# Kernel tuning notes

Measured on AMD Instinct MI355X. Metric: run time of the kernel, lower is better.

The kernel has to match this reference:

```python
import jax, jax.numpy as jnp
import numpy as np

H = 16          # num_heads
NB = 32         # pos_bias_num_buckets
EPS = 1e-8      # RMSNorm eps


def setup_inputs() -> dict:
    key = jax.random.key(0)
    ks = jax.random.split(key, 8)
    B, L, K, R, M, Dm, Dq = 2, 32, 2, 64, 128, 2048, 2048
    x = jax.random.normal(ks[0], (B, L, K, R, Dm), jnp.float32)
    past_ca_hidden_states = jax.random.normal(ks[1], (B, L, M, Dm), jnp.float32)
    past_ca_attention_mask = jax.random.bernoulli(ks[2], 0.95, (B, L, M)).astype(jnp.float32)
    ln_scale = jnp.ones((Dm,), jnp.float32)
    q_w = jax.random.normal(ks[3], (Dq, Dm), jnp.float32) * 0.02      # torch Linear weight [out,in]
    kv_w = jax.random.normal(ks[4], (2 * Dq, Dm), jnp.float32) * 0.02
    out_w = jax.random.normal(ks[5], (Dm, Dq), jnp.float32) * 0.02
    bias_table = jax.random.normal(ks[6], (NB, H), jnp.float32) * 0.02  # relative_attention_bias.weight
    return dict(x=x, past_ca_hidden_states=past_ca_hidden_states,
                past_ca_attention_mask=past_ca_attention_mask,
                ln_scale=ln_scale, q_w=q_w, kv_w=kv_w, out_w=out_w,
                bias_table=bias_table)


def _rel_bias(bias_table, r, m):
    # linear bucketing, bidirectional=True (RelativePositionBias._relative_position_bucket_linear)
    mn = -(NB // 2) - (NB % 2 - 1)   # -15 for NB=32
    mx = NB // 2                      # 16
    rel = jnp.arange(m)[None, :] - jnp.arange(r)[:, None]   # memory - query, [r, m]
    buckets = jnp.clip(rel, mn, mx) - mn                    # in [0, NB)
    return jnp.transpose(bias_table[buckets], (2, 0, 1))    # [H, r, m]


def reference(x, past_ca_hidden_states, past_ca_attention_mask,
              ln_scale, q_w, kv_w, out_w, bias_table):
    B, L, K, R, Dm = x.shape
    M = past_ca_hidden_states.shape[2]
    Dq = q_w.shape[0]
    dh = Dq // H

    # RMSNorm (p=-1: full norm)
    rms = jnp.linalg.norm(x, axis=-1, keepdims=True) * (Dm ** -0.5)
    xn = (x / (rms + EPS)) * ln_scale

    # projections (no bias)
    q = jnp.einsum('blkrc,qc->blkrq', xn, q_w)                 # [B,L,K,R,Dq]
    kv = jnp.einsum('blmc,qc->blmq', past_ca_hidden_states, kv_w)  # [B,L,M,2Dq]
    k = kv[..., :Dq]
    v = kv[..., Dq:]

    # split heads
    q = q.reshape(B, L, K, R, H, dh).transpose(0, 1, 2, 4, 3, 5)  # [B,L,K,H,R,dh]
    k = k.reshape(B, L, M, H, dh).transpose(0, 1, 3, 2, 4)        # [B,L,H,M,dh]
    v = v.reshape(B, L, M, H, dh).transpose(0, 1, 3, 2, 4)        # [B,L,H,M,dh]

    # NOTE: original applies NO 1/sqrt(dh) scaling
    scores = jnp.einsum('blkhrd,blhmd->blkhrm', q, k)             # [B,L,K,H,R,M]
    scores = scores + _rel_bias(bias_table, R, M)                 # broadcast [H,R,M]
    mask_add = (1.0 - past_ca_attention_mask) * -10000.0          # [B,L,M]
    scores = scores + mask_add[:, :, None, None, None, :]

    attn = jax.nn.softmax(scores, axis=-1)
    out = jnp.einsum('blkhrm,blhmd->blkhrd', attn, v)             # [B,L,K,H,R,dh]
    out = out.transpose(0, 1, 2, 4, 3, 5).reshape(B, L, K, R, Dq)  # merge heads '(h d)'
    out = jnp.einsum('blkrq,cq->blkrc', out, out_w)                # final_proj
    return out + x, attn
```

## Files before the change

### kernel.cpp

```cpp
#include <hip/hip_runtime.h>

typedef _Float16 f16;
typedef _Float16 f16x8 __attribute__((ext_vector_type(8)));
typedef float f32x4 __attribute__((ext_vector_type(4)));

#define LDS_GL16(g, l) __builtin_amdgcn_global_load_lds( \
    (const __attribute__((address_space(1))) void*)(g),  \
    (__attribute__((address_space(3))) void*)(l), 16, 0, 0)

__global__ __launch_bounds__(256) void conv_kern(const float* __restrict__ in,
                                                 f16* __restrict__ out, int n8) {
    int i = blockIdx.x * 256 + threadIdx.x;
    if (i >= n8) return;
    long o = (long)i * 8;
    float4 a = *(const float4*)(in + o);
    float4 b = *(const float4*)(in + o + 4);
    f16x8 v = { (f16)a.x,(f16)a.y,(f16)a.z,(f16)a.w,
                (f16)b.x,(f16)b.y,(f16)b.z,(f16)b.w };
    *(f16x8*)(out + o) = v;
}

__global__ __launch_bounds__(256) void rmsnorm_kern(const float* __restrict__ x,
                                                    const float* __restrict__ scale,
                                                    f16* __restrict__ out) {
    long base = (long)blockIdx.x * 2048 + threadIdx.x * 8;
    float4 a = *(const float4*)(x + base);
    float4 b = *(const float4*)(x + base + 4);
    float ss = a.x*a.x + a.y*a.y + a.z*a.z + a.w*a.w
             + b.x*b.x + b.y*b.y + b.z*b.z + b.w*b.w;
    #pragma unroll
    for (int d = 1; d < 64; d <<= 1) ss += __shfl_xor(ss, d, 64);
    __shared__ float red[4];
    if ((threadIdx.x & 63) == 0) red[threadIdx.x >> 6] = ss;
    __syncthreads();
    ss = red[0] + red[1] + red[2] + red[3];
    float inv = 1.0f / (sqrtf(ss * (1.0f / 2048.0f)) + 1e-8f);
    int c = threadIdx.x * 8;
    float4 s1 = *(const float4*)(scale + c);
    float4 s2 = *(const float4*)(scale + c + 4);
    f16x8 v = { (f16)(a.x*inv*s1.x),(f16)(a.y*inv*s1.y),(f16)(a.z*inv*s1.z),(f16)(a.w*inv*s1.w),
                (f16)(b.x*inv*s2.x),(f16)(b.y*inv*s2.y),(f16)(b.z*inv*s2.z),(f16)(b.w*inv*s2.w) };
    *(f16x8*)(out + base) = v;
}

template<int EPI>
__global__ __launch_bounds__(512, 2) void gemm256(
        const f16* __restrict__ A, const f16* __restrict__ B,
        f16* __restrict__ Ch, float* __restrict__ Cf,
        const float* __restrict__ resid, int M, int N, int Kd) {
    alignas(16) __shared__ f16 lds[65536];
    int nbx = N >> 8;
    int cpx = gridDim.x >> 3;
    int fid = (blockIdx.x & 7) * cpx + (blockIdx.x >> 3);
    int by = fid / nbx, bx = fid % nbx;
    int m0 = by << 8, n0 = bx << 8;
    int tid = threadIdx.x, lane = tid & 63, wid = tid >> 6;
    int wm = wid >> 2, wn = wid & 3, bh = wn >> 1;
    int lr = lane & 15, g = lane >> 4;

    long offA[4], offB[4]; int dA[4], dB[4];
    {
        int o16a = wn * 64 + lane;
        int o16b = ((wm << 1) | (wn & 1)) * 64 + lane;
        #pragma unroll
        for (int rd = 0; rd < 4; ++rd) {
            int oa = rd * 256 + o16a;
            int ra = wm * 128 + (oa >> 3);
            offA[rd] = (long)(m0 + ra) * Kd + (((lane & 7) ^ (ra & 7)) << 3);
            dA[rd] = wm * 8192 + oa * 8;
            int ob = rd * 256 + o16b;
            int rb = bh * 128 + (ob >> 3);
            offB[rd] = (long)(n0 + rb) * Kd + (((lane & 7) ^ (rb & 7)) << 3);
            dB[rd] = bh * 8192 + ob * 8;
        }
    }
    auto stage = [&](int kt, int p) {
        const f16* Ak = A + kt * 64;
        const f16* Bk = B + kt * 64;
        f16* la = lds + p * 16384;
        f16* lb = lds + 32768 + p * 16384;
        #pragma unroll
        for (int rd = 0; rd < 4; ++rd) {
            LDS_GL16(Ak + offA[rd], la + dA[rd]);
            LDS_GL16(Bk + offB[rd], lb + dB[rd]);
        }
    };

    f32x4 acc[8][4] = {};
    int NT = Kd >> 6;
    stage(0, 0);
    stage(1, 1);
    for (int t = 0; t < NT; ++t) {
        int p = t & 1;
        if (t + 1 < NT) asm volatile("s_waitcnt vmcnt(8)" ::: "memory");
        else            asm volatile("s_waitcnt vmcnt(0)" ::: "memory");
        __builtin_amdgcn_s_barrier();
        const f16* Ap = lds + p * 16384;
        const f16* Bp = lds + 32768 + p * 16384;
        f16x8 bf[2][4];
        #pragma unroll
        for (int kk = 0; kk < 2; ++kk)
            #pragma unroll
            for (int j = 0; j < 4; ++j) {
                int row = wn * 64 + j * 16 + lr;
                int c8 = (kk * 4 + g) ^ (row & 7);
                bf[kk][j] = *(const f16x8*)(Bp + row * 64 + c8 * 8);
            }
        #pragma unroll
        for (int q = 0; q < 4; ++q) {
            f16x8 af[2][2];
            #pragma unroll
            for (int kk = 0; kk < 2; ++kk)
                #pragma unroll
                for (int ii = 0; ii < 2; ++ii) {
                    int row = wm * 128 + (q * 2 + ii) * 16 + lr;
                    int c8 = (kk * 4 + g) ^ (row & 7);
                    af[kk][ii] = *(const f16x8*)(Ap + row * 64 + c8 * 8);
                }
            __builtin_amdgcn_s_setprio(1);
            #pragma unroll
            for (int ii = 0; ii < 2; ++ii)
                #pragma unroll
                for (int j = 0; j < 4; ++j)
                    #pragma unroll
                    for (int kk = 0; kk < 2; ++kk)
                        acc[q * 2 + ii][j] = __builtin_amdgcn_mfma_f32_16x16x32_f16(
                            af[kk][ii], bf[kk][j], acc[q * 2 + ii][j], 0, 0, 0);
            __builtin_amdgcn_s_setprio(0);
        }
        __builtin_amdgcn_s_barrier();
        if (t + 2 < NT) stage(t + 2, p);
    }
    #pragma unroll
    for (int i = 0; i < 8; ++i) {
        #pragma unroll
        for (int j = 0; j < 4; ++j) {
            #pragma unroll
            for (int reg = 0; reg < 4; ++reg) {
                int row = m0 + wm * 128 + i * 16 + g * 4 + reg;
                int col = n0 + wn * 64 + j * 16 + lr;
                long idx = (long)row * N + col;
                float v = acc[i][j][reg];
                if (EPI == 0) Ch[idx] = (f16)v;
                else          Cf[idx] = v + resid[idx];
            }
        }
    }
}

__global__ __launch_bounds__(256, 2) void attn_kern(
        const f16* __restrict__ Q,
        const f16* __restrict__ KV,
        const float* __restrict__ mask,
        const float* __restrict__ bias,
        float* __restrict__ attn_out,
        f16* __restrict__ pv_out) {
    __shared__ f16 Vs[128 * 128];
    __shared__ f16 P[64 * 136];
    int blk = blockIdx.x;
    int h  = blk & 15;
    int bk = blk >> 4;
    int bl = bk >> 1;
    int tid = threadIdx.x, lane = tid & 63, w = tid >> 6;
    int r0 = w << 4;
    int lr = lane & 15, g = lane >> 4;
    long qbase  = (long)bk * 64 * 2048;
    long kvbase = (long)bl * 128 * 4096;
    const f16* vsrc = KV + kvbase + 2048 + h * 128;
    {
        int idx = tid;
        #pragma unroll
        for (int rnd = 0; rnd < 8; ++rnd) {
            int vrow = idx >> 4, c = idx & 15;
            LDS_GL16(vsrc + (long)vrow * 4096 + c * 8, Vs + idx * 8);
            idx += 256;
        }
    }
    f16x8 aq[4];
    const f16* qrow = Q + qbase + (long)(r0 + lr) * 2048 + h * 128 + g * 8;
    #pragma unroll
    for (int t4 = 0; t4 < 4; ++t4) aq[t4] = *(const f16x8*)(qrow + t4 * 32);
    f32x4 s[8] = {};
    const f16* kbase = KV + kvbase + h * 128 + g * 8;
    #pragma unroll
    for (int j = 0; j < 8; ++j) {
        #pragma unroll
        for (int t4 = 0; t4 < 4; ++t4) {
            f16x8 bkf = *(const f16x8*)(kbase + (long)(j * 16 + lr) * 4096 + t4 * 32);
            s[j] = __builtin_amdgcn_mfma_f32_16x16x32_f16(aq[t4], bkf, s[j], 0, 0, 0);
        }
    }
    float madd[8];
    #pragma unroll
    for (int j = 0; j < 8; ++j)
        madd[j] = (1.0f - mask[(long)bl * 128 + j * 16 + lr]) * -10000.0f;
    #pragma unroll
    for (int reg = 0; reg < 4; ++reg) {
        int r = r0 + g * 4 + reg;
        float mx = -3.0e38f;
        #pragma unroll
        for (int j = 0; j < 8; ++j) {
            int m = j * 16 + lr;
            int rel = m - r;
            int bkt = (rel < -15 ? -15 : (rel > 16 ? 16 : rel)) + 15;
            float v = s[j][reg] + bias[bkt * 16 + h] + madd[j];
            s[j][reg] = v;
            mx = fmaxf(mx, v);
        }
        #pragma unroll
        for (int d = 1; d < 16; d <<= 1) mx = fmaxf(mx, __shfl_xor(mx, d, 64));
        float sum = 0.0f;
        #pragma unroll
        for (int j = 0; j < 8; ++j) {
            float e = __expf(s[j][reg] - mx);
            s[j][reg] = e;
            sum += e;
        }
        #pragma unroll
        for (int d = 1; d < 16; d <<= 1) sum += __shfl_xor(sum, d, 64);
        float inv = 1.0f / sum;
        #pragma unroll
        for (int j = 0; j < 8; ++j) s[j][reg] *= inv;
    }
    long abase = (long)blk * 64 * 128;
    #pragma unroll
    for (int reg = 0; reg < 4; ++reg) {
        int r = r0 + g * 4 + reg;
        #pragma unroll
        for (int j = 0; j < 8; ++j) {
            attn_out[abase + (long)r * 128 + j * 16 + lr] = s[j][reg];
            P[r * 136 + j * 16 + lr] = (f16)s[j][reg];
        }
    }
    __syncthreads();
    f16x8 pa[4];
    #pragma unroll
    for (int t4 = 0; t4 < 4; ++t4)
        pa[t4] = *(const f16x8*)(P + (r0 + lr) * 136 + t4 * 32 + g * 8);
    f32x4 o[8] = {};
    #pragma unroll
    for (int dj = 0; dj < 8; ++dj) {
        #pragma unroll
        for (int t4 = 0; t4 < 4; ++t4) {
            f16x8 bv;
            #pragma unroll
            for (int rg = 0; rg < 8; ++rg)
                bv[rg] = Vs[(t4 * 32 + g * 8 + rg) * 128 + dj * 16 + lr];
            o[dj] = __builtin_amdgcn_mfma_f32_16x16x32_f16(pa[t4], bv, o[dj], 0, 0, 0);
        }
    }
    f16* ob = pv_out + qbase + h * 128;
    #pragma unroll
    for (int dj = 0; dj < 8; ++dj)
        #pragma unroll
        for (int reg = 0; reg < 4; ++reg)
            ob[(long)(r0 + g * 4 + reg) * 2048 + dj * 16 + lr] = (f16)o[dj][reg];
}

extern "C" void kernel_launch(void* const* d_in, const int* in_sizes, int n_in,
                              void* d_out, int out_size, void* d_ws, size_t ws_size,
                              hipStream_t stream) {
    const float* x     = (const float*)d_in[0];
    const float* hid   = (const float*)d_in[1];
    const float* mask  = (const float*)d_in[2];
    const float* lnsc  = (const float*)d_in[3];
    const float* q_w   = (const float*)d_in[4];
    const float* kv_w  = (const float*)d_in[5];
    const float* out_w = (const float*)d_in[6];
    const float* bias  = (const float*)d_in[7];
    float* out0 = (float*)d_out;
    float* attn = out0 + 16777216;

    f16* kv_h  = (f16*)out0;
    f16* xn_h  = (f16*)attn;
    f16* hid_h = (f16*)(attn + 8388608);
    char* ws = (char*)d_ws;
    f16* q_h    = (f16*)(ws);
    f16* ao_h   = (f16*)(ws + 33554432L);
    f16* qw_h   = (f16*)(ws + 67108864L);
    f16* kvw_h  = (f16*)(ws + 75497472L);
    f16* outw_h = (f16*)(ws + 92274688L);

    conv_kern<<<2048, 256, 0, stream>>>(q_w,   qw_h,   524288);
    conv_kern<<<4096, 256, 0, stream>>>(kv_w,  kvw_h, 1048576);
    conv_kern<<<2048, 256, 0, stream>>>(out_w, outw_h, 524288);
    conv_kern<<<8192, 256, 0, stream>>>(hid,   hid_h, 2097152);
    rmsnorm_kern<<<8192, 256, 0, stream>>>(x, lnsc, xn_h);
    gemm256<0><<<256, 512, 0, stream>>>(xn_h, qw_h, q_h, nullptr, nullptr,
                                        8192, 2048, 2048);
    gemm256<0><<<512, 512, 0, stream>>>(hid_h, kvw_h, kv_h, nullptr, nullptr,
                                        8192, 4096, 2048);
    attn_kern<<<2048, 256, 0, stream>>>(q_h, kv_h, mask, bias, attn, ao_h);
    gemm256<1><<<256, 512, 0, stream>>>(ao_h, outw_h, nullptr, out0, x,
                                        8192, 2048, 2048);
}
```

Baseline: 424.4 us.

## Restructure GEMM main loop into 8-phase interleaved load/MFMA schedule

Rewrites the 256x256 GEMM main loop so each K-tile is split into quarter stages of global->LDS loads, interleaved with register-fragment loads and MFMA clusters across 8 barrier-separated phases per two K-tiles. This follows the HipKittens-style 8-wave ping-pong schedule and is meant to hide global and LDS latency behind matrix math. The price is many more barriers and a fixed-count vmcnt discipline, with a hand-written tail that assumes an even number of K-tiles.

```diff
diff --git a/kernel.cpp b/kernel.cpp
--- a/kernel.cpp
+++ b/kernel.cpp
@@ -7,6 +7,8 @@
 #define LDS_GL16(g, l) __builtin_amdgcn_global_load_lds( \
     (const __attribute__((address_space(1))) void*)(g),  \
     (__attribute__((address_space(3))) void*)(l), 16, 0, 0)
+#define VMCNT(N) asm volatile("s_waitcnt vmcnt(" #N ")" ::: "memory")
+#define BAR() __builtin_amdgcn_s_barrier()
 
 __global__ __launch_bounds__(256) void conv_kern(const float* __restrict__ in,
                                                  f16* __restrict__ out, int n8) {
@@ -54,83 +56,113 @@
     int fid = (blockIdx.x & 7) * cpx + (blockIdx.x >> 3);
     int by = fid / nbx, bx = fid % nbx;
     int m0 = by << 8, n0 = bx << 8;
-    int tid = threadIdx.x, lane = tid & 63, wid = tid >> 6;
-    int wm = wid >> 2, wn = wid & 3, bh = wn >> 1;
+    int tid = threadIdx.x, lane = tid & 63;
+    int wid = tid >> 6, wm = wid >> 2, wn = wid & 3;
     int lr = lane & 15, g = lane >> 4;
-
-    long offA[4], offB[4]; int dA[4], dB[4];
+    int iL = tid >> 3, cb = tid & 7;
+
+    auto stage = [&](int kt, int p, int r) {
+        #pragma unroll
+        for (int rnd = 0; rnd < 2; ++rnd) {
+            if (r == 0 || r == 3) {
+                int row = iL + rnd * 128 + (r == 3 ? 64 : 0);
+                LDS_GL16(A + (long)(m0 + row) * Kd + kt * 64 + ((cb ^ (row & 7)) << 3),
+                         lds + p * 16384 + row * 64 + (cb << 3));
+            } else {
+                int row = (iL & 31) + ((iL >> 5) + rnd * 2) * 64 + (r == 2 ? 32 : 0);
+                LDS_GL16(B + (long)(n0 + row) * Kd + kt * 64 + ((cb ^ (row & 7)) << 3),
+                         lds + 32768 + p * 16384 + row * 64 + (cb << 3));
+            }
+        }
+    };
+
+    f32x4 acc[8][4] = {};
+    f16x8 a[4][2], b0[2][2], b1[2][2];
+
+    auto loadA = [&](const f16* bp, int qm) {
+        #pragma unroll
+        for (int mf = 0; mf < 4; ++mf) {
+            int row = wm * 128 + (qm * 4 + mf) * 16 + lr;
+            #pragma unroll
+            for (int kk = 0; kk < 2; ++kk)
+                a[mf][kk] = *(const f16x8*)(bp + row * 64 + (((kk * 4 + g) ^ (row & 7)) << 3));
+        }
+    };
+    auto loadB = [&](f16x8 (&d)[2][2], const f16* bp, int qn) {
+        #pragma unroll
+        for (int nf = 0; nf < 2; ++nf) {
+            int row = wn * 64 + (qn * 2 + nf) * 16 + lr;
+            #pragma unroll
+            for (int kk = 0; kk < 2; ++kk)
+                d[nf][kk] = *(const f16x8*)(bp + row * 64 + (((kk * 4 + g) ^ (row & 7)) << 3));
+        }
+    };
+    auto mma = [&](f16x8 (&bb)[2][2], int qm, int qn) {
+        __builtin_amdgcn_s_setprio(1);
+        #pragma unroll
+        for (int mf = 0; mf < 4; ++mf)
+            #pragma unroll
+            for (int nf = 0; nf < 2; ++nf)
+                #pragma unroll
+                for (int kk = 0; kk < 2; ++kk)
+                    acc[qm * 4 + mf][qn * 2 + nf] = __builtin_amdgcn_mfma_f32_16x16x32_f16(
+                        a[mf][kk], bb[nf][kk], acc[qm * 4 + mf][qn * 2 + nf], 0, 0, 0);
+        __builtin_amdgcn_s_setprio(0);
+    };
+
+    const f16* A0p = lds;
+    const f16* A1p = lds + 16384;
+    const f16* B0p = lds + 32768;
+    const f16* B1p = lds + 49152;
+    int NT = Kd >> 6, NI = NT >> 1;
+
+    stage(0, 0, 0); stage(0, 0, 1); stage(0, 0, 2); stage(0, 0, 3);
+    stage(1, 1, 0); stage(1, 1, 1); stage(1, 1, 2);
+    VMCNT(6); BAR();
+
+    for (int it = 0; it < NI - 1; ++it) {
+        int t0 = it * 2;
+        loadA(A0p, 0); loadB(b0, B0p, 0);
+        stage(t0 + 1, 1, 3);
+        VMCNT(6); BAR(); mma(b0, 0, 0); BAR();
+        loadB(b1, B0p, 1);
+        stage(t0 + 2, 0, 0);
+        VMCNT(6); BAR(); mma(b1, 0, 1); BAR();
+        loadA(A0p, 1);
+        stage(t0 + 2, 0, 1);
+        VMCNT(6); BAR(); mma(b1, 1, 1); BAR();
+        stage(t0 + 2, 0, 2);
+        VMCNT(6); BAR(); mma(b0, 1, 0); BAR();
+        loadA(A1p, 0); loadB(b0, B1p, 0);
+        stage(t0 + 2, 0, 3);
+        VMCNT(6); BAR(); mma(b0, 0, 0); BAR();
+        loadB(b1, B1p, 1);
+        stage(t0 + 3, 1, 0);
+        VMCNT(6); BAR(); mma(b1, 0, 1); BAR();
+        loadA(A1p, 1);
+        stage(t0 + 3, 1, 1);
+        VMCNT(6); BAR(); mma(b1, 1, 1); BAR();
+        stage(t0 + 3, 1, 2);
+        VMCNT(6); BAR(); mma(b0, 1, 0); BAR();
+    }
     {
-        int o16a = wn * 64 + lane;
-        int o16b = ((wm << 1) | (wn & 1)) * 64 + lane;
-        #pragma unroll
-        for (int rd = 0; rd < 4; ++rd) {
-            int oa = rd * 256 + o16a;
-            int ra = wm * 128 + (oa >> 3);
-            offA[rd] = (long)(m0 + ra) * Kd + (((lane & 7) ^ (ra & 7)) << 3);
-            dA[rd] = wm * 8192 + oa * 8;
-            int ob = rd * 256 + o16b;
-            int rb = bh * 128 + (ob >> 3);
-            offB[rd] = (long)(n0 + rb) * Kd + (((lane & 7) ^ (rb & 7)) << 3);
-            dB[rd] = bh * 8192 + ob * 8;
-        }
-    }
-    auto stage = [&](int kt, int p) {
-        const f16* Ak = A + kt * 64;
-        const f16* Bk = B + kt * 64;
-        f16* la = lds + p * 16384;
-        f16* lb = lds + 32768 + p * 16384;
-        #pragma unroll
-        for (int rd = 0; rd < 4; ++rd) {
-            LDS_GL16(Ak + offA[rd], la + dA[rd]);
-            LDS_GL16(Bk + offB[rd], lb + dB[rd]);
-        }
-    };
-
-    f32x4 acc[8][4] = {};
-    int NT = Kd >> 6;
-    stage(0, 0);
-    stage(1, 1);
-    for (int t = 0; t < NT; ++t) {
-        int p = t & 1;
-        if (t + 1 < NT) asm volatile("s_waitcnt vmcnt(8)" ::: "memory");
-        else            asm volatile("s_waitcnt vmcnt(0)" ::: "memory");
-        __builtin_amdgcn_s_barrier();
-        const f16* Ap = lds + p * 16384;
-        const f16* Bp = lds + 32768 + p * 16384;
-        f16x8 bf[2][4];
-        #pragma unroll
-        for (int kk = 0; kk < 2; ++kk)
-            #pragma unroll
-            for (int j = 0; j < 4; ++j) {
-                int row = wn * 64 + j * 16 + lr;
-                int c8 = (kk * 4 + g) ^ (row & 7);
-                bf[kk][j] = *(const f16x8*)(Bp + row * 64 + c8 * 8);
-            }
-        #pragma unroll
-        for (int q = 0; q < 4; ++q) {
-            f16x8 af[2][2];
-            #pragma unroll
-            for (int kk = 0; kk < 2; ++kk)
-                #pragma unroll
-                for (int ii = 0; ii < 2; ++ii) {
-                    int row = wm * 128 + (q * 2 + ii) * 16 + lr;
-                    int c8 = (kk * 4 + g) ^ (row & 7);
-                    af[kk][ii] = *(const f16x8*)(Ap + row * 64 + c8 * 8);
-                }
-            __builtin_amdgcn_s_setprio(1);
-            #pragma unroll
-            for (int ii = 0; ii < 2; ++ii)
-                #pragma unroll
-                for (int j = 0; j < 4; ++j)
-                    #pragma unroll
-                    for (int kk = 0; kk < 2; ++kk)
-                        acc[q * 2 + ii][j] = __builtin_amdgcn_mfma_f32_16x16x32_f16(
-                            af[kk][ii], bf[kk][j], acc[q * 2 + ii][j], 0, 0, 0);
-            __builtin_amdgcn_s_setprio(0);
-        }
-        __builtin_amdgcn_s_barrier();
-        if (t + 2 < NT) stage(t + 2, p);
-    }
+        loadA(A0p, 0); loadB(b0, B0p, 0);
+        stage(NT - 1, 1, 3);
+        VMCNT(6); BAR(); mma(b0, 0, 0); BAR();
+        loadB(b1, B0p, 1);
+        VMCNT(6); BAR(); mma(b1, 0, 1); BAR();
+        loadA(A0p, 1);
+        VMCNT(6); BAR(); mma(b1, 1, 1); BAR();
+        VMCNT(4); BAR(); mma(b0, 1, 0); BAR();
+        loadA(A1p, 0); loadB(b0, B1p, 0);
+        VMCNT(2); BAR(); mma(b0, 0, 0); BAR();
+        loadB(b1, B1p, 1);
+        VMCNT(0); BAR(); mma(b1, 0, 1); BAR();
+        loadA(A1p, 1);
+        BAR(); mma(b1, 1, 1); BAR();
+        BAR(); mma(b0, 1, 0); BAR();
+    }
+
     #pragma unroll
     for (int i = 0; i < 8; ++i) {
         #pragma unroll
```

Result: faster. 403.7 us (-4.9%).
